# Kernel tuning notes

Measured on AMD Instinct MI355X. Metric: run time of the kernel, lower is better.

Reference implementation:

```python
import jax, jax.numpy as jnp
import numpy as np

N = 3072          # in_features == out_features (CIFAR-10 flat dim)
BATCH = 8192
K_TOP = 16        # K selected pseudo-diagonals
ALPHA_LR = 0.01   # l in the Dykstra soft top-k
NUM_ITER = 50


def sparse_soft_topk_mask_dykstra(alpha, k, l, num_iter=NUM_ITER):
    """Differentiable sparse top-k mask (Sander et al. 2023, p=2):
    Euclidean projection of alpha/l onto the capped simplex
    {m : 0 <= m <= 1, sum(m) = k}, via Dykstra's alternating projections
    (hyperplane sum=k  <->  box [0,1]^n). Returns exact zeros off the top-k.
    """
    z = alpha / l
    n = z.shape[0]

    def body(carry, _):
        x, p, q = carry
        # project x + p onto hyperplane {sum = k}
        y = x + p
        y = y + (k - jnp.sum(y)) / n
        p = x + p - y
        # project y + q onto box [0, 1]^n
        xn = jnp.clip(y + q, 0.0, 1.0)
        q = y + q - xn
        return (xn, p, q), None

    init = (z, jnp.zeros_like(z), jnp.zeros_like(z))
    (x, _, _), _ = jax.lax.scan(body, init, None, length=num_iter)
    return x


def setup_inputs() -> dict:
    key = jax.random.key(0)
    k1, k2, k3 = jax.random.split(key, 3)
    x = jax.random.normal(k1, (BATCH, N), dtype=jnp.float32)
    # kaiming_uniform_(a=sqrt(5)) on (N, N): bound = sqrt(6/((1+5)*N)) = 1/sqrt(N)
    limit = 1.0 / float(np.sqrt(N))
    V = jax.random.uniform(k2, (N, N), jnp.float32, -limit, limit)
    alpha = jax.random.uniform(k3, (N,), jnp.float32)  # alpha >= 0 as asserted
    return {"x": x, "V": V, "alpha": alpha}


def reference(x, V, alpha):
    n = V.shape[0]
    a_topk = sparse_soft_topk_mask_dykstra(alpha, K_TOP, ALPHA_LR)
    # Pseudo-diagonal mask for diag i: ones at (row=(i+c) % n, col=c).
    # matmul(mask_i, diag(V[i])) scales column c by V[i, c], so
    #   W[r, c] = sum_i a_topk[i] * V[i, c] * [r == (i + c) % n]
    # i.e. exactly one i contributes per (r, c): i = (r - c) mod n.
    # a_topk is exactly zero off the top-k, so this gather equals the
    # original loop over nonzero indices without materializing masks.
    r = jnp.arange(n)
    idx = (r[:, None] - r[None, :]) % n          # (in, out) -> source diag i
    W = a_topk[idx] * V[idx, r[None, :]]          # (in, out)
    # F.linear(x, W): x @ W.T, x: (B, out) -> out: (B, in)
    return x @ W.T
```

## Files before the change

### kernel.cpp

```cpp
#include <hip/hip_runtime.h>
#include <hip/hip_bf16.h>
#include <stdint.h>

#define NDIM 3072
#define BATCHN 8192
#define KTOP 16.0f
#define NITER 50

#define BM 128
#define BN 128
#define BK 32
#define NT (NDIM / BK)
#define SLOT_BYTES 16384
#define ABYTES 8192

typedef __attribute__((ext_vector_type(8))) short short8;
typedef __attribute__((ext_vector_type(4))) float floatx4;
typedef __attribute__((ext_vector_type(4))) unsigned short ushortx4;

__device__ inline unsigned short f2bf(float f) {
    __hip_bfloat16 h = __float2bfloat16(f);
    return *reinterpret_cast<unsigned short*>(&h);
}

__global__ void dykstra_kernel(const float* __restrict__ alpha, float* __restrict__ a_out) {
    const int lane = threadIdx.x;
    float z[48];
#pragma unroll
    for (int e = 0; e < 48; ++e) z[e] = alpha[e * 64 + lane] / 0.01f;
    float S = 0.f;
#pragma unroll
    for (int e = 0; e < 48; ++e) S += z[e];
#pragma unroll
    for (int m = 1; m < 64; m <<= 1) S += __shfl_xor(S, m, 64);

    float D = 0.f;
    for (int it = 0; it < NITER; ++it) {
        D += (KTOP - S) / (float)NDIM;
        float s2 = 0.f;
#pragma unroll
        for (int e = 0; e < 48; ++e) {
            float v = z[e] + D;
            v = v < 0.f ? 0.f : (v > 1.f ? 1.f : v);
            s2 += v;
        }
        S = s2;
#pragma unroll
        for (int m = 1; m < 64; m <<= 1) S += __shfl_xor(S, m, 64);
    }
#pragma unroll
    for (int e = 0; e < 48; ++e) {
        float v = z[e] + D;
        v = v < 0.f ? 0.f : (v > 1.f ? 1.f : v);
        a_out[e * 64 + lane] = v;
    }
}

__global__ __launch_bounds__(256) void build_w(const float* __restrict__ V,
                                               const float* __restrict__ a,
                                               unsigned short* __restrict__ W) {
    __shared__ float Vs[128][64];
    __shared__ float as_[128];
    const int tid = threadIdx.x;
    const int c0 = blockIdx.x * 64;
    const int r0 = blockIdx.y * 64;
    int ib = r0 - c0 - 63;
    ib %= NDIM; if (ib < 0) ib += NDIM;

    if (tid < 128) {
        int i = ib + tid; if (i >= NDIM) i -= NDIM;
        as_[tid] = a[i];
    }
#pragma unroll
    for (int it = 0; it < 8; ++it) {
        int idx = it * 256 + tid;
        int d = idx >> 4;
        int c4 = (idx & 15) * 4;
        int i = ib + d; if (i >= NDIM) i -= NDIM;
        *(floatx4*)&Vs[d][c4] = *(const floatx4*)&V[(size_t)i * NDIM + c0 + c4];
    }
    __syncthreads();

    const int c4 = (tid & 15) * 4;
    const int rr0 = tid >> 4;
#pragma unroll
    for (int p = 0; p < 4; ++p) {
        int rr = p * 16 + rr0;
        ushortx4 o;
#pragma unroll
        for (int j = 0; j < 4; ++j) {
            int cc = c4 + j;
            int d = rr - cc + 63;
            o[j] = f2bf(as_[d] * Vs[d][cc]);
        }
        *(ushortx4*)&W[(size_t)(r0 + rr) * NDIM + (c0 + c4)] = o;
    }
}

__global__ void convert_x(const float* __restrict__ x, unsigned short* __restrict__ xb, int n) {
    int i = (blockIdx.x * blockDim.x + threadIdx.x) * 4;
    const int stride = gridDim.x * blockDim.x * 4;
    for (; i < n; i += stride) {
        floatx4 v = *(const floatx4*)(x + i);
        ushortx4 o;
        o[0] = f2bf(v[0]); o[1] = f2bf(v[1]); o[2] = f2bf(v[2]); o[3] = f2bf(v[3]);
        *(ushortx4*)(xb + i) = o;
    }
}

__global__ __launch_bounds__(256, 2) void gemm_bt(const unsigned short* __restrict__ A,
                                                  const unsigned short* __restrict__ B,
                                                  float* __restrict__ C) {
    __shared__ __align__(16) char lds[4 * SLOT_BYTES];

    const int bid = blockIdx.x;
    const int swz = (bid & 7) * 192 + (bid >> 3);
    const int tm = swz & 63;
    const int tn = swz >> 6;
    const int m0 = tm * BM, n0 = tn * BN;

    const int tid = threadIdx.x;
    const int lane = tid & 63;
    const int wid = tid >> 6;
    const int wm = wid >> 1, wn = wid & 1;

    const unsigned short* Ab = A + (size_t)m0 * NDIM;
    const unsigned short* Bb = B + (size_t)n0 * NDIM;

    const int sblk = tid >> 6;
    const int srow = lane & 15;
    const int scol = (lane >> 4) * 8;

    floatx4 acc[4][4];
#pragma unroll
    for (int i = 0; i < 4; ++i)
#pragma unroll
        for (int j = 0; j < 4; ++j) acc[i][j] = {0.f, 0.f, 0.f, 0.f};

    auto STAGE = [&](int T) {
        char* sb = lds + (T & 3) * SLOT_BYTES;
        const int kt = T * BK;
#pragma unroll
        for (int r = 0; r < 2; ++r) {
            const unsigned short* g = Ab + (size_t)((r * 4 + sblk) * 16 + srow) * NDIM + kt + scol;
            __builtin_amdgcn_global_load_lds(
                (const __attribute__((address_space(1))) unsigned int*)g,
                (__attribute__((address_space(3))) unsigned int*)(sb + r * 4096 + tid * 16),
                16, 0, 0);
        }
#pragma unroll
        for (int r = 0; r < 2; ++r) {
            const unsigned short* g = Bb + (size_t)((r * 4 + sblk) * 16 + srow) * NDIM + kt + scol;
            __builtin_amdgcn_global_load_lds(
                (const __attribute__((address_space(1))) unsigned int*)g,
                (__attribute__((address_space(3))) unsigned int*)(sb + ABYTES + r * 4096 + tid * 16),
                16, 0, 0);
        }
    };

    STAGE(0); STAGE(1); STAGE(2);
    asm volatile("s_waitcnt vmcnt(8)" ::: "memory");
    asm volatile("s_barrier" ::: "memory");

    for (int T = 0; T < NT; ++T) {
        const char* sb = lds + (T & 3) * SLOT_BYTES;
        short8 af[4], bf[4];
#pragma unroll
        for (int mi = 0; mi < 4; ++mi)
            af[mi] = *(const short8*)(sb + (wm * 4 + mi) * 1024 + lane * 16);
#pragma unroll
        for (int ni = 0; ni < 4; ++ni)
            bf[ni] = *(const short8*)(sb + ABYTES + (wn * 4 + ni) * 1024 + lane * 16);

        if (T + 3 < NT) STAGE(T + 3);

        if (T < NT - 3)       { asm volatile("s_waitcnt vmcnt(8)" ::: "memory"); }
        else if (T == NT - 3) { asm volatile("s_waitcnt vmcnt(4)" ::: "memory"); }
        else if (T == NT - 2) { asm volatile("s_waitcnt vmcnt(0)" ::: "memory"); }
        asm volatile("s_barrier" ::: "memory");

        __builtin_amdgcn_s_setprio(1);
#pragma unroll
        for (int mi = 0; mi < 4; ++mi)
#pragma unroll
            for (int ni = 0; ni < 4; ++ni)
                acc[mi][ni] = __builtin_amdgcn_mfma_f32_16x16x32_bf16(af[mi], bf[ni], acc[mi][ni], 0, 0, 0);
        __builtin_amdgcn_s_setprio(0);
        asm volatile("s_barrier" ::: "memory");
    }

#pragma unroll
    for (int mi = 0; mi < 4; ++mi)
#pragma unroll
        for (int ni = 0; ni < 4; ++ni)
#pragma unroll
            for (int rg = 0; rg < 4; ++rg) {
                int rr = m0 + wm * 64 + mi * 16 + (lane >> 4) * 4 + rg;
                int cc = n0 + wn * 64 + ni * 16 + (lane & 15);
                C[(size_t)rr * NDIM + cc] = acc[mi][ni][rg];
            }
}

extern "C" void kernel_launch(void* const* d_in, const int* in_sizes, int n_in,
                              void* d_out, int out_size, void* d_ws, size_t ws_size,
                              hipStream_t stream) {
    const float* x     = (const float*)d_in[0];
    const float* V     = (const float*)d_in[1];
    const float* alpha = (const float*)d_in[2];
    float* out = (float*)d_out;

    float* a_ws = (float*)d_ws;
    unsigned short* xb = (unsigned short*)((char*)d_ws + 16384);
    unsigned short* Wb = (unsigned short*)((char*)d_ws + 16384 + (size_t)BATCHN * NDIM * 2);

    hipLaunchKernelGGL(dykstra_kernel, dim3(1), dim3(64), 0, stream, alpha, a_ws);
    hipLaunchKernelGGL(build_w, dim3(NDIM / 64, NDIM / 64), dim3(256), 0, stream, V, a_ws, Wb);
    hipLaunchKernelGGL(convert_x, dim3(2048), dim3(256), 0, stream, x, xb, BATCHN * NDIM);
    hipLaunchKernelGGL(gemm_bt, dim3((BATCHN / BM) * (NDIM / BN)), dim3(256), 0, stream,
                       xb, Wb, out);
}
```

Baseline: 523.2 us.

## Enlarge GEMM tile to 256x128x64 with 8 waves and triple-buffered split stages

The GEMM block tile grows to 256x128 with BK=64 and 512 threads (8 waves), and the pipeline changes from a 4-slot BK=32 ring to a 3-buffer ring of 48KB each. Each iteration splits the MFMA work into two halves over the N-subtiles and interleaves the global-to-LDS prefetch of tile t+2 between them. The larger tile raises arithmetic intensity and halves barrier count per unit of K. The cost is 144KB of LDS per block, which may limit occupancy to one block per CU despite the launch bounds, and higher register pressure.

```diff
diff --git a/kernel.cpp b/kernel.cpp
--- a/kernel.cpp
+++ b/kernel.cpp
@@ -7,12 +7,13 @@
 #define KTOP 16.0f
 #define NITER 50
 
-#define BM 128
+#define BM 256
 #define BN 128
-#define BK 32
-#define NT (NDIM / BK)
-#define SLOT_BYTES 16384
-#define ABYTES 8192
+#define BK 64
+#define NKT (NDIM / BK)
+#define A_BYTES 32768
+#define B_BYTES 16384
+#define BUF_BYTES 49152
 
 typedef __attribute__((ext_vector_type(8))) short short8;
 typedef __attribute__((ext_vector_type(4))) float floatx4;
@@ -108,28 +109,43 @@
     }
 }
 
-__global__ __launch_bounds__(256, 2) void gemm_bt(const unsigned short* __restrict__ A,
+__global__ __launch_bounds__(512, 2) void gemm_bt(const unsigned short* __restrict__ A,
                                                   const unsigned short* __restrict__ B,
                                                   float* __restrict__ C) {
-    __shared__ __align__(16) char lds[4 * SLOT_BYTES];
+    __shared__ __align__(16) char lds[3 * BUF_BYTES];
 
     const int bid = blockIdx.x;
-    const int swz = (bid & 7) * 192 + (bid >> 3);
-    const int tm = swz & 63;
-    const int tn = swz >> 6;
+    const int swz = (bid & 7) * 96 + (bid >> 3);
+    const int tm = swz / 24, tn = swz % 24;
     const int m0 = tm * BM, n0 = tn * BN;
 
     const int tid = threadIdx.x;
     const int lane = tid & 63;
     const int wid = tid >> 6;
-    const int wm = wid >> 1, wn = wid & 1;
+    const int wm = wid >> 1;
+    const int wn = wid & 1;
 
     const unsigned short* Ab = A + (size_t)m0 * NDIM;
     const unsigned short* Bb = B + (size_t)n0 * NDIM;
 
-    const int sblk = tid >> 6;
-    const int srow = lane & 15;
-    const int scol = (lane >> 4) * 8;
+    auto stageA = [&](char* sw, int kt, int i) {
+        int c = wid * 4 + i;
+        int b = c >> 1, kk = c & 1;
+        const unsigned short* g = Ab + (size_t)(b * 16 + (lane & 15)) * NDIM + kt + kk * 32 + (lane >> 4) * 8;
+        __builtin_amdgcn_global_load_lds(
+            (const __attribute__((address_space(1))) unsigned int*)g,
+            (__attribute__((address_space(3))) unsigned int*)(sw + c * 1024 + lane * 16),
+            16, 0, 0);
+    };
+    auto stageB = [&](char* sw, int kt, int i) {
+        int c = wid * 2 + i;
+        int b = c >> 1, kk = c & 1;
+        const unsigned short* g = Bb + (size_t)(b * 16 + (lane & 15)) * NDIM + kt + kk * 32 + (lane >> 4) * 8;
+        __builtin_amdgcn_global_load_lds(
+            (const __attribute__((address_space(1))) unsigned int*)g,
+            (__attribute__((address_space(3))) unsigned int*)(sw + A_BYTES + c * 1024 + lane * 16),
+            16, 0, 0);
+    };
 
     floatx4 acc[4][4];
 #pragma unroll
@@ -137,67 +153,84 @@
 #pragma unroll
         for (int j = 0; j < 4; ++j) acc[i][j] = {0.f, 0.f, 0.f, 0.f};
 
-    auto STAGE = [&](int T) {
-        char* sb = lds + (T & 3) * SLOT_BYTES;
-        const int kt = T * BK;
-#pragma unroll
-        for (int r = 0; r < 2; ++r) {
-            const unsigned short* g = Ab + (size_t)((r * 4 + sblk) * 16 + srow) * NDIM + kt + scol;
-            __builtin_amdgcn_global_load_lds(
-                (const __attribute__((address_space(1))) unsigned int*)g,
-                (__attribute__((address_space(3))) unsigned int*)(sb + r * 4096 + tid * 16),
-                16, 0, 0);
-        }
-#pragma unroll
-        for (int r = 0; r < 2; ++r) {
-            const unsigned short* g = Bb + (size_t)((r * 4 + sblk) * 16 + srow) * NDIM + kt + scol;
-            __builtin_amdgcn_global_load_lds(
-                (const __attribute__((address_space(1))) unsigned int*)g,
-                (__attribute__((address_space(3))) unsigned int*)(sb + ABYTES + r * 4096 + tid * 16),
-                16, 0, 0);
-        }
-    };
-
-    STAGE(0); STAGE(1); STAGE(2);
-    asm volatile("s_waitcnt vmcnt(8)" ::: "memory");
-    asm volatile("s_barrier" ::: "memory");
-
-    for (int T = 0; T < NT; ++T) {
-        const char* sb = lds + (T & 3) * SLOT_BYTES;
-        short8 af[4], bf[4];
-#pragma unroll
-        for (int mi = 0; mi < 4; ++mi)
-            af[mi] = *(const short8*)(sb + (wm * 4 + mi) * 1024 + lane * 16);
-#pragma unroll
-        for (int ni = 0; ni < 4; ++ni)
-            bf[ni] = *(const short8*)(sb + ABYTES + (wn * 4 + ni) * 1024 + lane * 16);
-
-        if (T + 3 < NT) STAGE(T + 3);
-
-        if (T < NT - 3)       { asm volatile("s_waitcnt vmcnt(8)" ::: "memory"); }
-        else if (T == NT - 3) { asm volatile("s_waitcnt vmcnt(4)" ::: "memory"); }
-        else if (T == NT - 2) { asm volatile("s_waitcnt vmcnt(0)" ::: "memory"); }
-        asm volatile("s_barrier" ::: "memory");
-
+    {
+        char* s0 = lds;
+        char* s1 = lds + BUF_BYTES;
+#pragma unroll
+        for (int i = 0; i < 4; ++i) stageA(s0, 0, i);
+        stageB(s0, 0, 0); stageB(s0, 0, 1);
+#pragma unroll
+        for (int i = 0; i < 4; ++i) stageA(s1, BK, i);
+        stageB(s1, BK, 0); stageB(s1, BK, 1);
+        asm volatile("s_waitcnt vmcnt(6)" ::: "memory");
+        asm volatile("s_barrier" ::: "memory");
+    }
+
+    int rb = 0;
+    for (int t = 0; t < NKT; ++t) {
+        const char* sb = lds + rb * BUF_BYTES;
+        int wbi = rb - 1; if (wbi < 0) wbi += 3;
+        char* sw = lds + wbi * BUF_BYTES;
+        const int kt2 = (t + 2) * BK;
+        const bool do_stage = (t + 2) < NKT;
+
+        short8 af[4][2], bf[2][2];
+#pragma unroll
+        for (int m = 0; m < 4; ++m)
+#pragma unroll
+            for (int kk = 0; kk < 2; ++kk)
+                af[m][kk] = *(const short8*)(sb + (wm * 4 + m) * 2048 + kk * 1024 + lane * 16);
+#pragma unroll
+        for (int n = 0; n < 2; ++n)
+#pragma unroll
+            for (int kk = 0; kk < 2; ++kk)
+                bf[n][kk] = *(const short8*)(sb + A_BYTES + (wn * 4 + n) * 2048 + kk * 1024 + lane * 16);
+        if (do_stage) { stageA(sw, kt2, 0); stageA(sw, kt2, 1); stageA(sw, kt2, 2); }
+        asm volatile("s_barrier" ::: "memory");
         __builtin_amdgcn_s_setprio(1);
 #pragma unroll
-        for (int mi = 0; mi < 4; ++mi)
-#pragma unroll
-            for (int ni = 0; ni < 4; ++ni)
-                acc[mi][ni] = __builtin_amdgcn_mfma_f32_16x16x32_bf16(af[mi], bf[ni], acc[mi][ni], 0, 0, 0);
+        for (int m = 0; m < 4; ++m)
+#pragma unroll
+            for (int n = 0; n < 2; ++n)
+#pragma unroll
+                for (int kk = 0; kk < 2; ++kk)
+                    acc[m][n] = __builtin_amdgcn_mfma_f32_16x16x32_bf16(af[m][kk], bf[n][kk], acc[m][n], 0, 0, 0);
         __builtin_amdgcn_s_setprio(0);
         asm volatile("s_barrier" ::: "memory");
-    }
-
-#pragma unroll
-    for (int mi = 0; mi < 4; ++mi)
-#pragma unroll
-        for (int ni = 0; ni < 4; ++ni)
+
+        short8 bg[2][2];
+#pragma unroll
+        for (int n = 0; n < 2; ++n)
+#pragma unroll
+            for (int kk = 0; kk < 2; ++kk)
+                bg[n][kk] = *(const short8*)(sb + A_BYTES + (wn * 4 + 2 + n) * 2048 + kk * 1024 + lane * 16);
+        if (do_stage) { stageA(sw, kt2, 3); stageB(sw, kt2, 0); stageB(sw, kt2, 1); }
+        asm volatile("s_barrier" ::: "memory");
+        __builtin_amdgcn_s_setprio(1);
+#pragma unroll
+        for (int m = 0; m < 4; ++m)
+#pragma unroll
+            for (int n = 0; n < 2; ++n)
+#pragma unroll
+                for (int kk = 0; kk < 2; ++kk)
+                    acc[m][2 + n] = __builtin_amdgcn_mfma_f32_16x16x32_bf16(af[m][kk], bg[n][kk], acc[m][2 + n], 0, 0, 0);
+        __builtin_amdgcn_s_setprio(0);
+        if (t + 2 < NKT)      { asm volatile("s_waitcnt vmcnt(6)" ::: "memory"); }
+        else if (t + 1 < NKT) { asm volatile("s_waitcnt vmcnt(0)" ::: "memory"); }
+        asm volatile("s_barrier" ::: "memory");
+
+        rb = rb + 1; if (rb == 3) rb = 0;
+    }
+
+#pragma unroll
+    for (int m = 0; m < 4; ++m)
+#pragma unroll
+        for (int n = 0; n < 4; ++n)
 #pragma unroll
             for (int rg = 0; rg < 4; ++rg) {
-                int rr = m0 + wm * 64 + mi * 16 + (lane >> 4) * 4 + rg;
-                int cc = n0 + wn * 64 + ni * 16 + (lane & 15);
-                C[(size_t)rr * NDIM + cc] = acc[mi][ni][rg];
+                int rr = m0 + wm * 64 + m * 16 + (lane >> 4) * 4 + rg;
+                int cc = n0 + wn * 64 + n * 16 + (lane & 15);
+                C[(size_t)rr * NDIM + cc] = acc[m][n][rg];
             }
 }
 
@@ -216,6 +249,6 @@
     hipLaunchKernelGGL(dykstra_kernel, dim3(1), dim3(64), 0, stream, alpha, a_ws);
     hipLaunchKernelGGL(build_w, dim3(NDIM / 64, NDIM / 64), dim3(256), 0, stream, V, a_ws, Wb);
     hipLaunchKernelGGL(convert_x, dim3(2048), dim3(256), 0, stream, x, xb, BATCHN * NDIM);
-    hipLaunchKernelGGL(gemm_bt, dim3((BATCHN / BM) * (NDIM / BN)), dim3(256), 0, stream,
+    hipLaunchKernelGGL(gemm_bt, dim3((BATCHN / BM) * (NDIM / BN)), dim3(512), 0, stream,
                        xb, Wb, out);
 }
```

Result: faster. 455.4 us (-12.9%).
